# Performance work log

Hardware: AMD Instinct MI355X
Metric: run time of the kernel (lower is better)

## Reference

```python
import jax, jax.numpy as jnp
import numpy as np

N = 100000
E = 1600000
D = 128  # out_dim == head_dim (num_heads = 1)


def setup_inputs() -> dict:
    key = jax.random.key(0)
    ks = jax.random.split(key, 16)
    s = 0.05
    inp = {
        "h": jax.random.normal(ks[0], (N, D), dtype=jnp.float32),
        "c": jax.random.normal(ks[1], (N, 3), dtype=jnp.float32),
        "src": jax.random.randint(ks[2], (E,), 0, N),
        "dst": jax.random.randint(ks[3], (E,), 0, N),
        # Q/K/V projections (use_bias=False)
        "Wq": jax.random.normal(ks[4], (D, D), dtype=jnp.float32) * s,
        "Wk": jax.random.normal(ks[5], (D, D), dtype=jnp.float32) * s,
        "Wv": jax.random.normal(ks[6], (D, D), dtype=jnp.float32) * s,
        # linear_p: Linear(3,3) -> ReLU -> Linear(3,D)
        "Wp1": jax.random.normal(ks[7], (3, 3), dtype=jnp.float32) * s,
        "bp1": jnp.zeros((3,), dtype=jnp.float32),
        "Wp2": jax.random.normal(ks[8], (3, D), dtype=jnp.float32) * s,
        "bp2": jnp.zeros((D,), dtype=jnp.float32),
        # edge MLP: Linear(D,D) -> ReLU -> Linear(D,1)
        "We1": jax.random.normal(ks[9], (D, D), dtype=jnp.float32) * s,
        "be1": jnp.zeros((D,), dtype=jnp.float32),
        "We2": jax.random.normal(ks[10], (D, 1), dtype=jnp.float32) * s,
        "be2": jnp.zeros((1,), dtype=jnp.float32),
        # output projection O (has bias)
        "Wo": jax.random.normal(ks[11], (D, D), dtype=jnp.float32) * s,
        "bo": jnp.zeros((D,), dtype=jnp.float32),
    }
    return inp


def reference(h, c, src, dst, Wq, Wk, Wv, Wp1, bp1, Wp2, bp2,
              We1, be1, We2, be2, Wo, bo):
    scale = np.sqrt(np.float32(D))  # sqrt(out_dim) used by scaled_exp
    n = h.shape[0]
    # node projections
    Q = h @ Wq                                   # [N, D]
    K = h @ Wk                                   # [N, D]
    V = h @ Wv                                   # [N, D]
    P = jax.nn.relu(c @ Wp1 + bp1) @ Wp2 + bp2   # [N, D] position encoding
    # per-edge point-transformer score: MLP(K[src] - Q[dst] + P[src])
    dif = K[src] - Q[dst] + P[src]               # [E, D]
    raw = jax.nn.relu(dif @ We1 + be1) @ We2 + be2  # [E, 1]
    score = jnp.exp(jnp.clip(raw / scale, -5.0, 5.0))  # [E, 1]
    # gather-multiply-scatter: weighted V+P sum and normalizer z per dst node
    msg = (V + P)[src] * score                   # [E, D]
    wV = jax.ops.segment_sum(msg, dst, num_segments=n)    # [N, D]
    z = jax.ops.segment_sum(score, dst, num_segments=n)   # [N, 1]
    head_out = wV / z                            # [N, D]
    return head_out @ Wo + bo                    # [N, D]
```

## Files before the change

kernel.cpp:

```cpp
#include <hip/hip_runtime.h>
#include <math.h>

#define DD 128
#define CAP 10240
typedef unsigned int u32;
typedef unsigned short u16;
typedef __attribute__((ext_vector_type(8))) short bf16x8;
typedef __attribute__((ext_vector_type(4))) float f32x4;
typedef __attribute__((ext_vector_type(2))) float f32x2;

__device__ __forceinline__ float4 f4zero() { return make_float4(0.f, 0.f, 0.f, 0.f); }
__device__ __forceinline__ u32 bf16rne(float f) {
    u32 u = __float_as_uint(f);
    u += 0x7FFFu + ((u >> 16) & 1u);
    return u >> 16;
}
__device__ __forceinline__ u32 pack2(float lo, float hi) {
    return bf16rne(lo) | (bf16rne(hi) << 16);
}
__device__ __forceinline__ float unlo(u32 u) { return __uint_as_float(u << 16); }
__device__ __forceinline__ float unhi(u32 u) { return __uint_as_float(u & 0xFFFF0000u); }

__global__ __launch_bounds__(256) void fused_pre(
    const float* __restrict__ Wq, const float* __restrict__ Wk,
    const float* __restrict__ Wv, const float* __restrict__ We1,
    const float* __restrict__ be1, const float* __restrict__ Wp2,
    const float* __restrict__ bp2, const float* __restrict__ Wo,
    u32* __restrict__ BF,
    const int* __restrict__ src, const int* __restrict__ dst,
    int* __restrict__ gcount, u32* __restrict__ ebuf, int E) {
    const int t = threadIdx.x;
    if (blockIdx.x < 38) {
        const int bid = blockIdx.x * 4 + (t >> 6);
        const int l = t & 63;
        const int c = l & 15;
        const int kg = l >> 4;
        float val[8];

        if (bid < 120) {
            const int ct = bid / 5, ks = bid - ct * 5;
            const int u = ct / 6, r = ct - u * 6;
            const int n = 32 * u + 16 * (r < 2 ? r : (r & 1)) + c;
#pragma unroll
            for (int j = 0; j < 8; ++j) {
                const int k = ks * 32 + kg * 8 + j;
                float v = 0.f;
                if (r < 2) {
                    if (k < 128) {
                        float a = 0.f;
                        for (int q = 0; q < 128; ++q)
                            a = fmaf(Wq[k * 128 + q], We1[q * 128 + n], a);
                        v = a;
                    }
                } else if (r < 4) {
                    if (k < 128) {
                        float a = 0.f;
                        for (int q = 0; q < 128; ++q)
                            a = fmaf(Wk[k * 128 + q], We1[q * 128 + n], a);
                        v = a;
                    } else if (k < 131) {
                        float a = 0.f;
                        for (int q = 0; q < 128; ++q)
                            a = fmaf(Wp2[(k - 128) * 128 + q], We1[q * 128 + n], a);
                        v = a;
                    } else if (k == 131) {
                        float a = be1[n];
                        for (int q = 0; q < 128; ++q)
                            a = fmaf(bp2[q], We1[q * 128 + n], a);
                        v = a;
                    }
                } else {
                    if (k < 128) v = Wv[k * 128 + n];
                    else if (k < 131) v = Wp2[(k - 128) * 128 + n];
                    else if (k == 131) v = bp2[n];
                }
                val[j] = v;
            }
        } else {
            const int b2 = bid - 120;
            const int ct = b2 >> 2, ks = b2 & 3;
            const int n = ct * 16 + c;
#pragma unroll
            for (int j = 0; j < 8; ++j) {
                const int k = ks * 32 + kg * 8 + j;
                val[j] = Wo[k * 128 + n];
            }
        }
        u32* dp = &BF[((size_t)bid * 64 + l) * 4];
        dp[0] = pack2(val[0], val[1]);
        dp[1] = pack2(val[2], val[3]);
        dp[2] = pack2(val[4], val[5]);
        dp[3] = pack2(val[6], val[7]);
    } else {
        __shared__ int hist[256];
        __shared__ int base[256];
        hist[t] = 0;
        __syncthreads();
        const int chunk = (blockIdx.x - 38) * 4096;
        int bk[16], rk[16];
        u32 pv[16];
#pragma unroll
        for (int i = 0; i < 16; ++i) {
            int idx = chunk + i * 256 + t;
            bk[i] = -1;
            if (idx < E) {
                int dd = dst[idx];
                int ss = src[idx];
                bk[i] = dd >> 9;
                pv[i] = ((u32)ss << 9) | (u32)(dd & 511);
                rk[i] = atomicAdd(&hist[bk[i]], 1);
            }
        }
        __syncthreads();
        if (hist[t]) base[t] = t * CAP + atomicAdd(&gcount[t], hist[t]);
        __syncthreads();
#pragma unroll
        for (int i = 0; i < 16; ++i) {
            if (bk[i] >= 0) ebuf[base[bk[i]] + rk[i]] = pv[i];
        }
    }
}

__global__ __launch_bounds__(256) void scanB_we2r(
    const int* __restrict__ gcount, int* __restrict__ bucket_base,
    const float* __restrict__ We2, float* __restrict__ We2r) {
    __shared__ int s[256];
    int t = threadIdx.x;
    int orig = gcount[t];
    s[t] = orig;
    __syncthreads();
    for (int off = 1; off < 256; off <<= 1) {
        int x = (t >= off) ? s[t - off] : 0;
        __syncthreads();
        s[t] += x;
        __syncthreads();
    }
    bucket_base[t] = s[t] - orig;
    if (t < 128) {
        int col = 32 * (t >> 5) + 16 * (t & 1) + ((t & 31) >> 1);
        We2r[t] = We2[col];
    }
}

__global__ __launch_bounds__(256) void fused_mid(
    const float* __restrict__ h, const float* __restrict__ c,
    const float* __restrict__ Wp1, const float* __restrict__ bp1,
    const u32* __restrict__ BF,
    u32* __restrict__ QWb, u32* __restrict__ Vb,
    unsigned char* __restrict__ Kb8, int N,
    const int* __restrict__ gcount, const int* __restrict__ bucket_base,
    const u32* __restrict__ ebuf, int* __restrict__ ssrc,
    int* __restrict__ offs, int E, int NR) {
    __shared__ u32 lds[64 * 96];
    const int t = threadIdx.x;

    if ((int)blockIdx.x < NR) {
        int* cnt = (int*)lds;
        int* cur = cnt + 512;
        int* ts = cur + 512;
        const int r = blockIdx.x;
        const int cnt_r = gcount[r];
        const int base_r = bucket_base[r];
        cnt[t] = 0;
        cnt[t + 256] = 0;
        __syncthreads();
        const u32* eb = &ebuf[(size_t)r * CAP];
        for (int i = t; i < cnt_r; i += 256) atomicAdd(&cnt[eb[i] & 511], 1);
        __syncthreads();
        int v0 = cnt[2 * t], v1 = cnt[2 * t + 1];
        int pair = v0 + v1;
        ts[t] = pair;
        __syncthreads();
        for (int off = 1; off < 256; off <<= 1) {
            int x = (t >= off) ? ts[t - off] : 0;
            __syncthreads();
            ts[t] += x;
            __syncthreads();
        }
        int ex = ts[t] - pair;
        cur[2 * t] = ex;
        cur[2 * t + 1] = ex + v0;
        offs[r * 512 + 2 * t] = base_r + ex;
        offs[r * 512 + 2 * t + 1] = base_r + ex + v0;
        if (r == NR - 1 && t == 255) offs[NR * 512] = E;
        __syncthreads();
        for (int i = t; i < cnt_r; i += 256) {
            u32 e = eb[i];
            int p = atomicAdd(&cur[e & 511], 1);
            ssrc[base_r + p] = (int)(e >> 9);
        }
    } else {
        u32* hs = lds;
        const int row0 = ((int)blockIdx.x - NR) * 64;

#pragma unroll
        for (int i = 0; i < 8; ++i) {
            int f = t + i * 256;
            int row = f >> 5;
            int cq = f & 31;
            float4 v = f4zero();
            if (row0 + row < N) v = *(const float4*)&h[(size_t)(row0 + row) * DD + cq * 4];
            int idx = row * 96 + ((cq * 2) ^ ((row & 7) << 2));
            uint2 p;
            p.x = pack2(v.x, v.y);
            p.y = pack2(v.z, v.w);
            *(uint2*)&hs[idx] = p;
        }
        if (t < 64) {
            int row = t;
            float u0 = 0.f, u1 = 0.f, u2 = 0.f;
            if (row0 + row < N) {
                const float* cr = &c[(size_t)(row0 + row) * 3];
                float c0 = cr[0], c1 = cr[1], c2 = cr[2];
                u0 = fmaxf(bp1[0] + c0 * Wp1[0] + c1 * Wp1[3] + c2 * Wp1[6], 0.f);
                u1 = fmaxf(bp1[1] + c0 * Wp1[1] + c1 * Wp1[4] + c2 * Wp1[7], 0.f);
                u2 = fmaxf(bp1[2] + c0 * Wp1[2] + c1 * Wp1[5] + c2 * Wp1[8], 0.f);
            }
            int swz = (row & 7) << 2;
            uint4 z0 = make_uint4(pack2(u0, u1), pack2(u2, 1.0f), 0u, 0u);
            uint4 zz = make_uint4(0u, 0u, 0u, 0u);
#pragma unroll
            for (int q = 0; q < 4; ++q) {
                int idx = row * 96 + 64 + ((q * 4) ^ swz);
                *(uint4*)&hs[idx] = (q == 0) ? z0 : zz;
            }
        }
        __syncthreads();

        const int w = t >> 6, l = t & 63;
        const int cc = l & 15, kg = l >> 4;

        f32x4 acc[4][6];
#pragma unroll
        for (int rt = 0; rt < 4; ++rt)
#pragma unroll
            for (int r = 0; r < 6; ++r) acc[rt][r] = (f32x4){0.f, 0.f, 0.f, 0.f};

#pragma unroll
        for (int ks = 0; ks < 5; ++ks) {
            bf16x8 a[4];
#pragma unroll
            for (int rt = 0; rt < 4; ++rt) {
                int row = rt * 16 + cc;
                int idx = row * 96 + ((ks * 16 + kg * 4) ^ ((row & 7) << 2));
                a[rt] = *(const bf16x8*)&hs[idx];
            }
#pragma unroll
            for (int r = 0; r < 6; ++r) {
                const bf16x8 b = *(const bf16x8*)&BF[(((size_t)(w * 6 + r) * 5 + ks) * 64 + l) * 4];
#pragma unroll
                for (int rt = 0; rt < 4; ++rt)
                    acc[rt][r] = __builtin_amdgcn_mfma_f32_16x16x32_bf16(a[rt], b, acc[rt][r], 0, 0, 0);
            }
        }

#pragma unroll
        for (int rt = 0; rt < 4; ++rt) {
#pragma unroll
            for (int j = 0; j < 4; ++j) {
                int row = row0 + rt * 16 + kg * 4 + j;
                if (row >= N) continue;
                QWb[(size_t)row * 64 + w * 16 + cc] = pack2(acc[rt][0][j], acc[rt][1][j]);
                Vb[(size_t)row * 64 + w * 16 + cc] = pack2(acc[rt][4][j], acc[rt][5][j]);
                u32 kp = __builtin_amdgcn_cvt_pk_fp8_f32(acc[rt][2][j], acc[rt][3][j], 0u, false);
                *(u16*)&Kb8[(size_t)row * 128 + w * 32 + cc * 2] = (u16)kp;
            }
        }
    }
}

__global__ __launch_bounds__(256) void aggregate(
    const int* __restrict__ offs, const int* __restrict__ ssrc,
    const unsigned char* __restrict__ Kb8, const u32* __restrict__ Vb,
    const u32* __restrict__ QWb, const float* __restrict__ We2r,
    const float* __restrict__ be2, u32* __restrict__ headb, int N) {
    const int node = (blockIdx.x * 256 + threadIdx.x) >> 6;
    const int lane = threadIdx.x & 63;
    if (node >= N) return;
    const int g = lane >> 4, i = lane & 15;

    const float SC = 0.08838834764831845f * 1.4426950408889634f;
    const float CL = 5.0f * 1.4426950408889634f;

    uint4 Qu = *(const uint4*)&QWb[(size_t)node * 64 + 4 * i];
    float q0 = unlo(Qu.x), q1 = unhi(Qu.x), q2 = unlo(Qu.y), q3 = unhi(Qu.y);
    float q4 = unlo(Qu.z), q5 = unhi(Qu.z), q6 = unlo(Qu.w), q7 = unhi(Qu.w);
    float4 wA = *(const float4*)&We2r[8 * i];
    float4 wB = *(const float4*)&We2r[8 * i + 4];
    float b2 = be2[0];

    const int beg = offs[node], end = offs[node + 1];
    float a0 = 0.f, a1 = 0.f, a2 = 0.f, a3 = 0.f;
    float a4 = 0.f, a5 = 0.f, a6 = 0.f, a7 = 0.f;
    float zacc = 0.f;

    int s0 = (beg + g < end) ? ssrc[beg + g] : 0;
    int s1 = (beg + 4 + g < end) ? ssrc[beg + 4 + g] : 0;
    uint2 kk = *(const uint2*)&Kb8[(size_t)s0 * 128 + 8 * i];
    uint4 va = *(const uint4*)&Vb[(size_t)s0 * 64 + 4 * i];

    for (int e0 = beg; e0 < end; e0 += 4) {
        const bool act = (e0 + g) < end;
        const uint2 kkc = kk;
        const uint4 vac = va;

        int en2 = e0 + 8 + g;
        int s2 = (en2 < end) ? ssrc[en2] : 0;
        kk = *(const uint2*)&Kb8[(size_t)s1 * 128 + 8 * i];
        va = *(const uint4*)&Vb[(size_t)s1 * 64 + 4 * i];
        s1 = s2;

        f32x2 f0 = __builtin_amdgcn_cvt_pk_f32_fp8(kkc.x, false);
        f32x2 f1 = __builtin_amdgcn_cvt_pk_f32_fp8(kkc.x, true);
        f32x2 f2 = __builtin_amdgcn_cvt_pk_f32_fp8(kkc.y, false);
        f32x2 f3 = __builtin_amdgcn_cvt_pk_f32_fp8(kkc.y, true);

        float p;
        p = fmaxf(f0[0] - q0, 0.f) * wA.x;
        p = fmaf(fmaxf(f0[1] - q1, 0.f), wA.y, p);
        p = fmaf(fmaxf(f1[0] - q2, 0.f), wA.z, p);
        p = fmaf(fmaxf(f1[1] - q3, 0.f), wA.w, p);
        p = fmaf(fmaxf(f2[0] - q4, 0.f), wB.x, p);
        p = fmaf(fmaxf(f2[1] - q5, 0.f), wB.y, p);
        p = fmaf(fmaxf(f3[0] - q6, 0.f), wB.z, p);
        p = fmaf(fmaxf(f3[1] - q7, 0.f), wB.w, p);
#pragma unroll
        for (int off = 1; off <= 8; off <<= 1) p += __shfl_xor(p, off);

        float targ = (p + b2) * SC;
        targ = fminf(fmaxf(targ, -CL), CL);
        float sc = act ? exp2f(targ) : 0.f;

        a0 = fmaf(unlo(vac.x), sc, a0);
        a1 = fmaf(unhi(vac.x), sc, a1);
        a2 = fmaf(unlo(vac.y), sc, a2);
        a3 = fmaf(unhi(vac.y), sc, a3);
        a4 = fmaf(unlo(vac.z), sc, a4);
        a5 = fmaf(unhi(vac.z), sc, a5);
        a6 = fmaf(unlo(vac.w), sc, a6);
        a7 = fmaf(unhi(vac.w), sc, a7);
        zacc += sc;
    }

    a0 += __shfl_xor(a0, 16); a0 += __shfl_xor(a0, 32);
    a1 += __shfl_xor(a1, 16); a1 += __shfl_xor(a1, 32);
    a2 += __shfl_xor(a2, 16); a2 += __shfl_xor(a2, 32);
    a3 += __shfl_xor(a3, 16); a3 += __shfl_xor(a3, 32);
    a4 += __shfl_xor(a4, 16); a4 += __shfl_xor(a4, 32);
    a5 += __shfl_xor(a5, 16); a5 += __shfl_xor(a5, 32);
    a6 += __shfl_xor(a6, 16); a6 += __shfl_xor(a6, 32);
    a7 += __shfl_xor(a7, 16); a7 += __shfl_xor(a7, 32);
    zacc += __shfl_xor(zacc, 16); zacc += __shfl_xor(zacc, 32);

    if (g == 0) {
        float rz = 1.0f / zacc;
        uint4 o;
        o.x = pack2(a0 * rz, a1 * rz);
        o.y = pack2(a2 * rz, a3 * rz);
        o.z = pack2(a4 * rz, a5 * rz);
        o.w = pack2(a6 * rz, a7 * rz);
        *(uint4*)&headb[(size_t)node * 64 + 4 * i] = o;
    }
}

__global__ __launch_bounds__(256) void out_mfma(
    const u32* __restrict__ headb, const u32* __restrict__ WoF,
    const float* __restrict__ bo, float* __restrict__ out, int N) {
    __shared__ u32 hs[64 * 64];

    const int row0 = blockIdx.x * 64;
    const int t = threadIdx.x;

#pragma unroll
    for (int i = 0; i < 4; ++i) {
        int f = t + i * 256;
        int row = f >> 4;
        int cq = f & 15;
        uint4 v = make_uint4(0u, 0u, 0u, 0u);
        if (row0 + row < N) v = *(const uint4*)&headb[(size_t)(row0 + row) * 64 + cq * 4];
        int m = cq >> 2;
        int cb = (cq & 3) * 4;
        int swz = (row & 7) << 2;
        uint2 A, B;
        A.x = (v.x & 0xFFFFu) | (v.y << 16);
        A.y = (v.z & 0xFFFFu) | (v.w << 16);
        B.x = (v.x >> 16) | (v.y & 0xFFFF0000u);
        B.y = (v.z >> 16) | (v.w & 0xFFFF0000u);
        int dA = 16 * m + (cb >> 1);
        *(uint2*)&hs[row * 64 + (dA ^ swz)] = A;
        *(uint2*)&hs[row * 64 + ((dA + 8) ^ swz)] = B;
    }
    __syncthreads();

    const int w = t >> 6, l = t & 63;
    const int cc = l & 15, kg = l >> 4;

    f32x4 acc[4][2];
#pragma unroll
    for (int rt = 0; rt < 4; ++rt) {
        acc[rt][0] = (f32x4){0.f, 0.f, 0.f, 0.f};
        acc[rt][1] = (f32x4){0.f, 0.f, 0.f, 0.f};
    }

#pragma unroll
    for (int ks = 0; ks < 4; ++ks) {
        bf16x8 a[4];
#pragma unroll
        for (int rt = 0; rt < 4; ++rt) {
            int row = rt * 16 + cc;
            int idx = row * 64 + ((ks * 16 + kg * 4) ^ ((row & 7) << 2));
            a[rt] = *(const bf16x8*)&hs[idx];
        }
#pragma unroll
        for (int ctl = 0; ctl < 2; ++ctl) {
            const bf16x8 b = *(const bf16x8*)&WoF[(((size_t)(2 * w + ctl) * 4 + ks) * 64 + l) * 4];
#pragma unroll
            for (int rt = 0; rt < 4; ++rt)
                acc[rt][ctl] = __builtin_amdgcn_mfma_f32_16x16x32_bf16(a[rt], b, acc[rt][ctl], 0, 0, 0);
        }
    }

#pragma unroll
    for (int ctl = 0; ctl < 2; ++ctl) {
        int col = (2 * w + ctl) * 16 + cc;
        float bias = bo[col];
#pragma unroll
        for (int rt = 0; rt < 4; ++rt) {
#pragma unroll
            for (int j = 0; j < 4; ++j) {
                int row = row0 + rt * 16 + kg * 4 + j;
                if (row >= N) continue;
                out[(size_t)row * DD + col] = acc[rt][ctl][j] + bias;
            }
        }
    }
}

extern "C" void kernel_launch(void* const* d_in, const int* in_sizes, int n_in,
                              void* d_out, int out_size, void* d_ws, size_t ws_size,
                              hipStream_t stream) {
    const float* h   = (const float*)d_in[0];
    const float* c   = (const float*)d_in[1];
    const int*   src = (const int*)d_in[2];
    const int*   dst = (const int*)d_in[3];
    const float* Wq  = (const float*)d_in[4];
    const float* Wk  = (const float*)d_in[5];
    const float* Wv  = (const float*)d_in[6];
    const float* Wp1 = (const float*)d_in[7];
    const float* bp1 = (const float*)d_in[8];
    const float* Wp2 = (const float*)d_in[9];
    const float* bp2 = (const float*)d_in[10];
    const float* We1 = (const float*)d_in[11];
    const float* be1 = (const float*)d_in[12];
    const float* We2 = (const float*)d_in[13];
    const float* be2 = (const float*)d_in[14];
    const float* Wo  = (const float*)d_in[15];
    const float* bo  = (const float*)d_in[16];

    const int N = in_sizes[0] / DD;
    const int E = in_sizes[2];
    const int NR = (N + 511) >> 9;
    const int NB1 = (E + 4095) / 4096;
    const int NG = (N + 63) / 64;

    u32* BF    = (u32*)d_ws;
    u32* WoF   = BF + 120 * 256;
    u32* QWb   = BF + 152 * 256;
    u32* Vb    = QWb + (size_t)N * 64;
    unsigned char* Kb8 = (unsigned char*)(Vb + (size_t)N * 64);
    u32* headb = (u32*)(Kb8 + (size_t)N * 128);
    int* offs  = (int*)(headb + (size_t)N * 64);
    int* gcount = offs + ((size_t)NR * 512 + 1);
    int* bbase  = gcount + 256;
    float* We2r = (float*)(bbase + 256);
    int* ssrc   = (int*)(We2r + 128);
    u32* ebuf   = (u32*)(ssrc + E);

    hipMemsetAsync(gcount, 0, 256 * sizeof(int), stream);

    fused_pre<<<38 + NB1, 256, 0, stream>>>(Wq, Wk, Wv, We1, be1, Wp2, bp2, Wo,
                                            BF, src, dst, gcount, ebuf, E);

    scanB_we2r<<<1, 256, 0, stream>>>(gcount, bbase, We2, We2r);

    fused_mid<<<NR + NG, 256, 0, stream>>>(
        h, c, Wp1, bp1, BF, QWb, Vb, Kb8, N,
        gcount, bbase, ebuf, ssrc, offs, E, NR);

    aggregate<<<(N * 64 + 255) / 256, 256, 0, stream>>>(offs, ssrc, Kb8, Vb,
                                                        QWb, We2r, be2, headb, N);

    out_mfma<<<NG, 256, 0, stream>>>(headb, WoF, bo, (float*)d_out, N);
}
```

Baseline: 212.7 us.

## Interleave fp8 K and bf16 V rows and use packed math in aggregation

K (fp8) and V (bf16) per node now live in one 384-byte row, so each gathered edge source reads one contiguous region instead of two separate arrays. The aggregate loop drops the two-deep K/V register prefetch and keeps only a one-ahead prefetch of the source index. The score and accumulation math is rewritten with 2-wide float vectors so the compiler can emit packed FMA/max instructions, and the bias is folded into a single fma. The risk is less latency hiding for the irregular gathers, which occupancy alone has to cover.

Result: no change. 211.2 us (-0.7%).

```diff
diff --git a/kernel.cpp b/kernel.cpp
--- a/kernel.cpp
+++ b/kernel.cpp
@@ -146,8 +146,7 @@
     const float* __restrict__ h, const float* __restrict__ c,
     const float* __restrict__ Wp1, const float* __restrict__ bp1,
     const u32* __restrict__ BF,
-    u32* __restrict__ QWb, u32* __restrict__ Vb,
-    unsigned char* __restrict__ Kb8, int N,
+    u32* __restrict__ QWb, unsigned char* __restrict__ KV, int N,
     const int* __restrict__ gcount, const int* __restrict__ bucket_base,
     const u32* __restrict__ ebuf, int* __restrict__ ssrc,
     int* __restrict__ offs, int E, int NR) {
@@ -261,9 +260,10 @@
                 int row = row0 + rt * 16 + kg * 4 + j;
                 if (row >= N) continue;
                 QWb[(size_t)row * 64 + w * 16 + cc] = pack2(acc[rt][0][j], acc[rt][1][j]);
-                Vb[(size_t)row * 64 + w * 16 + cc] = pack2(acc[rt][4][j], acc[rt][5][j]);
+                unsigned char* kvrow = &KV[(size_t)row * 384];
                 u32 kp = __builtin_amdgcn_cvt_pk_fp8_f32(acc[rt][2][j], acc[rt][3][j], 0u, false);
-                *(u16*)&Kb8[(size_t)row * 128 + w * 32 + cc * 2] = (u16)kp;
+                *(u16*)&kvrow[w * 32 + cc * 2] = (u16)kp;
+                *(u32*)&kvrow[128 + 4 * (w * 16 + cc)] = pack2(acc[rt][4][j], acc[rt][5][j]);
             }
         }
     }
@@ -271,9 +271,9 @@
 
 __global__ __launch_bounds__(256) void aggregate(
     const int* __restrict__ offs, const int* __restrict__ ssrc,
-    const unsigned char* __restrict__ Kb8, const u32* __restrict__ Vb,
-    const u32* __restrict__ QWb, const float* __restrict__ We2r,
-    const float* __restrict__ be2, u32* __restrict__ headb, int N) {
+    const unsigned char* __restrict__ KV, const u32* __restrict__ QWb,
+    const float* __restrict__ We2r, const float* __restrict__ be2,
+    u32* __restrict__ headb, int N) {
     const int node = (blockIdx.x * 256 + threadIdx.x) >> 6;
     const int lane = threadIdx.x & 63;
     if (node >= N) return;
@@ -283,64 +283,63 @@
     const float CL = 5.0f * 1.4426950408889634f;
 
     uint4 Qu = *(const uint4*)&QWb[(size_t)node * 64 + 4 * i];
-    float q0 = unlo(Qu.x), q1 = unhi(Qu.x), q2 = unlo(Qu.y), q3 = unhi(Qu.y);
-    float q4 = unlo(Qu.z), q5 = unhi(Qu.z), q6 = unlo(Qu.w), q7 = unhi(Qu.w);
-    float4 wA = *(const float4*)&We2r[8 * i];
-    float4 wB = *(const float4*)&We2r[8 * i + 4];
-    float b2 = be2[0];
+    f32x2 q01 = {unlo(Qu.x), unhi(Qu.x)};
+    f32x2 q23 = {unlo(Qu.y), unhi(Qu.y)};
+    f32x2 q45 = {unlo(Qu.z), unhi(Qu.z)};
+    f32x2 q67 = {unlo(Qu.w), unhi(Qu.w)};
+    f32x2 w01 = *(const f32x2*)&We2r[8 * i];
+    f32x2 w23 = *(const f32x2*)&We2r[8 * i + 2];
+    f32x2 w45 = *(const f32x2*)&We2r[8 * i + 4];
+    f32x2 w67 = *(const f32x2*)&We2r[8 * i + 6];
+    const float B2SC = be2[0] * SC;
+    const f32x2 zero2 = {0.f, 0.f};
 
     const int beg = offs[node], end = offs[node + 1];
-    float a0 = 0.f, a1 = 0.f, a2 = 0.f, a3 = 0.f;
-    float a4 = 0.f, a5 = 0.f, a6 = 0.f, a7 = 0.f;
+    f32x2 acc01 = zero2, acc23 = zero2, acc45 = zero2, acc67 = zero2;
     float zacc = 0.f;
 
-    int s0 = (beg + g < end) ? ssrc[beg + g] : 0;
-    int s1 = (beg + 4 + g < end) ? ssrc[beg + 4 + g] : 0;
-    uint2 kk = *(const uint2*)&Kb8[(size_t)s0 * 128 + 8 * i];
-    uint4 va = *(const uint4*)&Vb[(size_t)s0 * 64 + 4 * i];
-
+    int e = beg + g;
+    int s = (e < end) ? ssrc[e] : 0;
     for (int e0 = beg; e0 < end; e0 += 4) {
         const bool act = (e0 + g) < end;
-        const uint2 kkc = kk;
-        const uint4 vac = va;
-
-        int en2 = e0 + 8 + g;
-        int s2 = (en2 < end) ? ssrc[en2] : 0;
-        kk = *(const uint2*)&Kb8[(size_t)s1 * 128 + 8 * i];
-        va = *(const uint4*)&Vb[(size_t)s1 * 64 + 4 * i];
-        s1 = s2;
-
-        f32x2 f0 = __builtin_amdgcn_cvt_pk_f32_fp8(kkc.x, false);
-        f32x2 f1 = __builtin_amdgcn_cvt_pk_f32_fp8(kkc.x, true);
-        f32x2 f2 = __builtin_amdgcn_cvt_pk_f32_fp8(kkc.y, false);
-        f32x2 f3 = __builtin_amdgcn_cvt_pk_f32_fp8(kkc.y, true);
-
-        float p;
-        p = fmaxf(f0[0] - q0, 0.f) * wA.x;
-        p = fmaf(fmaxf(f0[1] - q1, 0.f), wA.y, p);
-        p = fmaf(fmaxf(f1[0] - q2, 0.f), wA.z, p);
-        p = fmaf(fmaxf(f1[1] - q3, 0.f), wA.w, p);
-        p = fmaf(fmaxf(f2[0] - q4, 0.f), wB.x, p);
-        p = fmaf(fmaxf(f2[1] - q5, 0.f), wB.y, p);
-        p = fmaf(fmaxf(f3[0] - q6, 0.f), wB.z, p);
-        p = fmaf(fmaxf(f3[1] - q7, 0.f), wB.w, p);
+        const unsigned char* row = &KV[(size_t)s * 384];
+        uint2 kk = *(const uint2*)&row[8 * i];
+        uint4 vv = *(const uint4*)&row[128 + 16 * i];
+        int en = e0 + 4 + g;
+        s = (en < end) ? ssrc[en] : 0;
+
+        f32x2 d, p2;
+        d = __builtin_amdgcn_cvt_pk_f32_fp8(kk.x, false) - q01;
+        d = __builtin_elementwise_max(d, zero2);
+        p2 = d * w01;
+        d = __builtin_amdgcn_cvt_pk_f32_fp8(kk.x, true) - q23;
+        d = __builtin_elementwise_max(d, zero2);
+        p2 += d * w23;
+        d = __builtin_amdgcn_cvt_pk_f32_fp8(kk.y, false) - q45;
+        d = __builtin_elementwise_max(d, zero2);
+        p2 += d * w45;
+        d = __builtin_amdgcn_cvt_pk_f32_fp8(kk.y, true) - q67;
+        d = __builtin_elementwise_max(d, zero2);
+        p2 += d * w67;
+        float p = p2[0] + p2[1];
 #pragma unroll
         for (int off = 1; off <= 8; off <<= 1) p += __shfl_xor(p, off);
 
-        float targ = (p + b2) * SC;
+        float targ = fmaf(p, SC, B2SC);
         targ = fminf(fmaxf(targ, -CL), CL);
         float sc = act ? exp2f(targ) : 0.f;
-
-        a0 = fmaf(unlo(vac.x), sc, a0);
-        a1 = fmaf(unhi(vac.x), sc, a1);
-        a2 = fmaf(unlo(vac.y), sc, a2);
-        a3 = fmaf(unhi(vac.y), sc, a3);
-        a4 = fmaf(unlo(vac.z), sc, a4);
-        a5 = fmaf(unhi(vac.z), sc, a5);
-        a6 = fmaf(unlo(vac.w), sc, a6);
-        a7 = fmaf(unhi(vac.w), sc, a7);
+        f32x2 sc2 = {sc, sc};
+
+        f32x2 v;
+        v = (f32x2){unlo(vv.x), unhi(vv.x)}; acc01 += v * sc2;
+        v = (f32x2){unlo(vv.y), unhi(vv.y)}; acc23 += v * sc2;
+        v = (f32x2){unlo(vv.z), unhi(vv.z)}; acc45 += v * sc2;
+        v = (f32x2){unlo(vv.w), unhi(vv.w)}; acc67 += v * sc2;
         zacc += sc;
     }
+
+    float a0 = acc01[0], a1 = acc01[1], a2 = acc23[0], a3 = acc23[1];
+    float a4 = acc45[0], a5 = acc45[1], a6 = acc67[0], a7 = acc67[1];
 
     a0 += __shfl_xor(a0, 16); a0 += __shfl_xor(a0, 32);
     a1 += __shfl_xor(a1, 16); a1 += __shfl_xor(a1, 32);
@@ -466,9 +465,8 @@
     u32* BF    = (u32*)d_ws;
     u32* WoF   = BF + 120 * 256;
     u32* QWb   = BF + 152 * 256;
-    u32* Vb    = QWb + (size_t)N * 64;
-    unsigned char* Kb8 = (unsigned char*)(Vb + (size_t)N * 64);
-    u32* headb = (u32*)(Kb8 + (size_t)N * 128);
+    unsigned char* KV = (unsigned char*)(QWb + (size_t)N * 64);
+    u32* headb = (u32*)(KV + (size_t)N * 384);
     int* offs  = (int*)(headb + (size_t)N * 64);
     int* gcount = offs + ((size_t)NR * 512 + 1);
     int* bbase  = gcount + 256;
@@ -484,11 +482,11 @@
     scanB_we2r<<<1, 256, 0, stream>>>(gcount, bbase, We2, We2r);
 
     fused_mid<<<NR + NG, 256, 0, stream>>>(
-        h, c, Wp1, bp1, BF, QWb, Vb, Kb8, N,
+        h, c, Wp1, bp1, BF, QWb, KV, N,
         gcount, bbase, ebuf, ssrc, offs, E, NR);
 
-    aggregate<<<(N * 64 + 255) / 256, 256, 0, stream>>>(offs, ssrc, Kb8, Vb,
-                                                        QWb, We2r, be2, headb, N);
+    aggregate<<<(N * 64 + 255) / 256, 256, 0, stream>>>(offs, ssrc, KV, QWb,
+                                                        We2r, be2, headb, N);
 
     out_mfma<<<NG, 256, 0, stream>>>(headb, WoF, bo, (float*)d_out, N);
 }
```
